# Optimization experiments

Measured on AMD Instinct MI355X. Metric: run time of the kernel, lower is better.

## Reference

```python
import jax, jax.numpy as jnp
import numpy as np

NUM_HEADS = 16
NEG_INF = -1e24


def setup_inputs() -> dict:
    key = jax.random.key(0)
    k1, k2, k3, k4 = jax.random.split(key, 4)
    T, B, E = 2048, 2, 1024
    std = 0.02
    return {
        "x": jax.random.normal(k1, (T, B, E), dtype=jnp.float32),
        "in_proj_weight": jax.random.normal(k2, (3 * E, E), dtype=jnp.float32) * std,
        "in_proj_bias": jnp.zeros((3 * E,), dtype=jnp.float32),
        "out_w": jax.random.normal(k3, (E, E), dtype=jnp.float32) * std,
        "out_b": jnp.zeros((E,), dtype=jnp.float32),
        "key_padding_mask": jax.random.randint(k4, (T, B), 0, 2) > 0,
    }


def reference(x, in_proj_weight, in_proj_bias, out_w, out_b, key_padding_mask):
    # x: [T, B, E]  (Time x Batch x Channel), self-attention (qkv_same path)
    T, B, E = x.shape
    H = NUM_HEADS
    hd = E // H
    scaling = hd ** -0.5
    qkv = jnp.einsum("tbe,fe->tbf", x, in_proj_weight) + in_proj_bias  # [T,B,3E]
    q, k, v = jnp.split(qkv, 3, axis=-1)
    q = (q * scaling).reshape(T, B, H, hd)
    k = k.reshape(T, B, H, hd)
    v = v.reshape(T, B, H, hd)
    # attention scores: [B, H, T(tgt), S(src)]
    scores = jnp.einsum("tbhd,sbhd->bhts", q, k)
    # key_padding_mask: [S, B] -> broadcast over [B, 1, 1, S]
    pad = key_padding_mask.T[:, None, None, :]
    scores = jnp.where(pad, jnp.float32(NEG_INF), scores)
    attn_weights = jax.nn.softmax(scores, axis=-1)
    # dropout p=0.0 in eval -> identity
    attn = jnp.einsum("bhts,sbhd->tbhd", attn_weights, v).reshape(T, B, E)
    out = jnp.einsum("tbe,fe->tbf", attn, out_w) + out_b
    return out
```

## Files before the change

### kernel.cpp

```cpp
#include <hip/hip_runtime.h>
#include <math.h>

#define T_    2048
#define B_    2
#define E_    1024
#define H_    16
#define HD_   64
#define KD_   1024
#define N3_   3072
#define M_    4096
#define NEGI  -1e24f

typedef __attribute__((ext_vector_type(8))) short          bf16x8;
typedef __attribute__((ext_vector_type(4))) float          f32x4;
typedef __attribute__((ext_vector_type(8))) unsigned short u16x8;

__device__ __forceinline__ unsigned short f2bf(float x) {
    unsigned int u = __float_as_uint(x);
    return (unsigned short)((u + 0x7fffu + ((u >> 16) & 1u)) >> 16);
}

__device__ __forceinline__ unsigned int cvtpk_bf16(float a, float b) {
    unsigned int r;
    asm("v_cvt_pk_bf16_f32 %0, %1, %2" : "=v"(r) : "v"(a), "v"(b));
    return r;
}

__device__ __forceinline__ void gload16(const unsigned short* g, unsigned short* s) {
    __builtin_amdgcn_global_load_lds(
        (const __attribute__((address_space(1))) void*)g,
        (__attribute__((address_space(3))) void*)s, 16, 0, 0);
}

#define XN4  ((size_t)M_ * KD_ / 4)
#define WIN4 ((size_t)N3_ * KD_ / 4)
#define WON4 ((size_t)E_ * KD_ / 4)
__global__ __launch_bounds__(256) void cvt_all(const float* __restrict__ x,
                                               const float* __restrict__ wi,
                                               const float* __restrict__ wo,
                                               unsigned short* __restrict__ dst) {
    const size_t i = (size_t)blockIdx.x * 256 + threadIdx.x;
    const float* s; size_t off;
    if (i < XN4)             { s = x;  off = i; }
    else if (i < XN4 + WIN4) { s = wi; off = i - XN4; }
    else                     { s = wo; off = i - XN4 - WIN4; }
    float4 v = ((const float4*)s)[off];
    ushort4 o;
    o.x = f2bf(v.x); o.y = f2bf(v.y); o.z = f2bf(v.z); o.w = f2bf(v.w);
    ((ushort4*)dst)[i] = o;
}

__global__ __launch_bounds__(256) void build_msk(const int* __restrict__ m,
                                                 float* __restrict__ o) {
    int i = blockIdx.x * 256 + threadIdx.x;
    if (i >= T_ * B_) return;
    o[(i & 1) * T_ + (i >> 1)] = m[i] ? NEGI : 0.f;
}

template <int EPI>
__global__ __launch_bounds__(256) void gemm_mfma(
    const unsigned short* __restrict__ A, const unsigned short* __restrict__ W,
    const float* __restrict__ bias,
    unsigned short* __restrict__ q_o, unsigned short* __restrict__ k_o,
    unsigned short* __restrict__ v_o, float* __restrict__ f_o)
{
    __shared__ __align__(16) unsigned short Ab[128 * 64];
    __shared__ __align__(16) unsigned short Bb[128 * 64];
    const int tid = threadIdx.x;
    const int l = tid & 63, w = tid >> 6;
    const int lr = l & 15, g = l >> 4;
    const int m0 = blockIdx.y * 128, n0 = blockIdx.x * 128;
    const int wr = (w >> 1) * 64, wc = (w & 1) * 64;

    f32x4 acc[4][4];
    #pragma unroll
    for (int i = 0; i < 4; ++i)
        #pragma unroll
        for (int j = 0; j < 4; ++j) acc[i][j] = f32x4{0.f, 0.f, 0.f, 0.f};

    for (int k0 = 0; k0 < KD_; k0 += 64) {
        __syncthreads();
        #pragma unroll
        for (int i = 0; i < 4; ++i) {
            const int fb  = (i * 4 + w) * 64;
            const int row = (fb + l) >> 3;
            const int col = ((l & 7) ^ (row & 7)) * 8;
            gload16(&A[(size_t)(m0 + row) * KD_ + k0 + col], &Ab[fb * 8]);
            gload16(&W[(size_t)(n0 + row) * KD_ + k0 + col], &Bb[fb * 8]);
        }
        __syncthreads();
        #pragma unroll
        for (int ks = 0; ks < 2; ++ks) {
            bf16x8 af[4], bf[4];
            #pragma unroll
            for (int mi = 0; mi < 4; ++mi) {
                const int row = wr + mi * 16 + lr;
                af[mi] = *(const bf16x8*)&Ab[row * 64 + (((ks * 4 + g) ^ (row & 7)) * 8)];
            }
            #pragma unroll
            for (int ni = 0; ni < 4; ++ni) {
                const int row = wc + ni * 16 + lr;
                bf[ni] = *(const bf16x8*)&Bb[row * 64 + (((ks * 4 + g) ^ (row & 7)) * 8)];
            }
            #pragma unroll
            for (int mi = 0; mi < 4; ++mi)
                #pragma unroll
                for (int ni = 0; ni < 4; ++ni)
                    acc[mi][ni] = __builtin_amdgcn_mfma_f32_16x16x32_bf16(
                        af[mi], bf[ni], acc[mi][ni], 0, 0, 0);
        }
    }

    if (EPI == 0) {
        const int sec = n0 >> 10;
        unsigned short* dst = (sec == 0) ? q_o : (sec == 1) ? k_o : v_o;
        const float sc = (sec == 0) ? 0.125f : 1.f;
        #pragma unroll
        for (int ni = 0; ni < 4; ++ni) {
            const int fcol = n0 + wc + ni * 16 + lr;
            const int h = (fcol >> 6) & 15, d = fcol & 63;
            const float bv = bias[fcol];
            #pragma unroll
            for (int mi = 0; mi < 4; ++mi)
                #pragma unroll
                for (int p = 0; p < 4; ++p) {
                    const int m = m0 + wr + mi * 16 + g * 4 + p;
                    const int t = m >> 1, b = m & 1;
                    dst[((size_t)(b * H_ + h) * T_ + t) * HD_ + d] =
                        f2bf((acc[mi][ni][p] + bv) * sc);
                }
        }
    } else {
        #pragma unroll
        for (int ni = 0; ni < 4; ++ni) {
            const int fcol = n0 + wc + ni * 16 + lr;
            const float bv = bias[fcol];
            #pragma unroll
            for (int mi = 0; mi < 4; ++mi)
                #pragma unroll
                for (int p = 0; p < 4; ++p) {
                    const int m = m0 + wr + mi * 16 + g * 4 + p;
                    f_o[(size_t)m * E_ + fcol] = acc[mi][ni][p] + bv;
                }
        }
    }
}

__global__ __launch_bounds__(256) void transpose64(const unsigned short* __restrict__ v,
                                                   unsigned short* __restrict__ vt)
{
    __shared__ __align__(16) unsigned short tile[64][72];
    const int bh = blockIdx.y, t0 = blockIdx.x * 64;
    const int tid = threadIdx.x;
    const int r = tid >> 2, c0 = (tid & 3) * 16;
    const unsigned short* src = v + ((size_t)bh * T_ + t0 + r) * HD_ + c0;
    *(u16x8*)&tile[r][c0]     = *(const u16x8*)&src[0];
    *(u16x8*)&tile[r][c0 + 8] = *(const u16x8*)&src[8];
    __syncthreads();
    u16x8 a, b;
    #pragma unroll
    for (int j = 0; j < 8; ++j) a[j] = tile[c0 + j][r];
    #pragma unroll
    for (int j = 0; j < 8; ++j) b[j] = tile[c0 + 8 + j][r];
    unsigned short* dq = vt + ((size_t)bh * HD_ + r) * T_ + t0 + c0;
    *(u16x8*)&dq[0] = a;
    *(u16x8*)&dq[8] = b;
}

__device__ __forceinline__ void stage8(const unsigned short* src, int ld,
                                       unsigned short* buf, int w, int l) {
    const int fb  = w * 64;
    const int row = (fb + l) >> 3;
    const int col = ((l & 7) ^ (row & 7)) * 8;
    gload16(src + (size_t)row * ld + col, buf + fb * 8);
}

__global__ __launch_bounds__(512, 2) void attn_mfma(
    const unsigned short* __restrict__ qw, const unsigned short* __restrict__ kw,
    const unsigned short* __restrict__ vtw, const float* __restrict__ msk,
    unsigned short* __restrict__ attn)
{
    __shared__ __align__(16) unsigned short Kb[2][64 * 64];
    __shared__ __align__(16) unsigned short Vb[2][64 * 64];
    __shared__ __align__(16) unsigned short Pb[8][32 * 64];

    const int tid = threadIdx.x;
    const int l = tid & 63, w = tid >> 6;
    const int lr = l & 15, g = l >> 4;
    const int bh = blockIdx.y, b = bh >> 4, h = bh & 15;
    const int q0 = blockIdx.x * 256 + w * 32;

    const unsigned short* kb  = kw  + (size_t)bh * T_ * HD_;
    const unsigned short* vtb = vtw + (size_t)bh * HD_ * T_;
    const float* mb = msk + b * T_;
    unsigned short* Pw = Pb[w];

    bf16x8 qf[2][2];
    #pragma unroll
    for (int qc = 0; qc < 2; ++qc) {
        const unsigned short* qrow = qw + ((size_t)bh * T_ + q0 + qc * 16 + lr) * HD_;
        qf[qc][0] = *(const bf16x8*)&qrow[g * 8];
        qf[qc][1] = *(const bf16x8*)&qrow[32 + g * 8];
    }

    f32x4 o[2][4];
    #pragma unroll
    for (int qc = 0; qc < 2; ++qc)
        #pragma unroll
        for (int df = 0; df < 4; ++df) o[qc][df] = f32x4{0.f, 0.f, 0.f, 0.f};
    float m_run[2] = {-INFINITY, -INFINITY}, l_run[2] = {0.f, 0.f};

    stage8(kb, HD_, Kb[0], w, l);
    stage8(vtb, T_, Vb[0], w, l);
    int cur = 0;

    for (int s0 = 0; s0 < T_; s0 += 64) {
        __syncthreads();
        if (s0 + 64 < T_) {
            stage8(kb + (size_t)(s0 + 64) * HD_, HD_, Kb[cur ^ 1], w, l);
            stage8(vtb + (s0 + 64),          T_, Vb[cur ^ 1], w, l);
        }
        const unsigned short* Kc = Kb[cur];
        const unsigned short* Vc = Vb[cur];

        f32x4 st[4][2];
        #pragma unroll
        for (int sf = 0; sf < 4; ++sf) {
            const int row = sf * 16 + lr;
            const bf16x8 k0v = *(const bf16x8*)&Kc[row * 64 + ((g       ^ (row & 7)) * 8)];
            const bf16x8 k1v = *(const bf16x8*)&Kc[row * 64 + (((4 + g) ^ (row & 7)) * 8)];
            #pragma unroll
            for (int qc = 0; qc < 2; ++qc) {
                f32x4 z = f32x4{0.f, 0.f, 0.f, 0.f};
                z           = __builtin_amdgcn_mfma_f32_16x16x32_bf16(k0v, qf[qc][0], z, 0, 0, 0);
                st[sf][qc]  = __builtin_amdgcn_mfma_f32_16x16x32_bf16(k1v, qf[qc][1], z, 0, 0, 0);
            }
        }
        float4 mv[4];
        #pragma unroll
        for (int sf = 0; sf < 4; ++sf) mv[sf] = *(const float4*)&mb[s0 + sf * 16 + g * 4];

        #pragma unroll
        for (int qc = 0; qc < 2; ++qc) {
            float pmax = -INFINITY;
            #pragma unroll
            for (int sf = 0; sf < 4; ++sf) {
                st[sf][qc][0] += mv[sf].x; st[sf][qc][1] += mv[sf].y;
                st[sf][qc][2] += mv[sf].z; st[sf][qc][3] += mv[sf].w;
                pmax = fmaxf(pmax, fmaxf(fmaxf(st[sf][qc][0], st[sf][qc][1]),
                                         fmaxf(st[sf][qc][2], st[sf][qc][3])));
            }
            pmax = fmaxf(pmax, __shfl_xor(pmax, 16));
            pmax = fmaxf(pmax, __shfl_xor(pmax, 32));
            if (!__all(pmax - m_run[qc] <= 8.f)) {
                const float mnew = fmaxf(m_run[qc], pmax);
                const float fac  = __expf(m_run[qc] - mnew);
                l_run[qc] *= fac;
                #pragma unroll
                for (int df = 0; df < 4; ++df) {
                    o[qc][df][0] *= fac; o[qc][df][1] *= fac;
                    o[qc][df][2] *= fac; o[qc][df][3] *= fac;
                }
                m_run[qc] = mnew;
            }
            const float mcur = m_run[qc];
            float rsum = 0.f;
            unsigned int pk[8];
            #pragma unroll
            for (int sf = 0; sf < 4; ++sf) {
                const float e0 = __expf(st[sf][qc][0] - mcur), e1 = __expf(st[sf][qc][1] - mcur);
                const float e2 = __expf(st[sf][qc][2] - mcur), e3 = __expf(st[sf][qc][3] - mcur);
                rsum += (e0 + e1) + (e2 + e3);
                pk[sf * 2 + 0] = cvtpk_bf16(e0, e1);
                pk[sf * 2 + 1] = cvtpk_bf16(e2, e3);
            }
            rsum += __shfl_xor(rsum, 16);
            rsum += __shfl_xor(rsum, 32);
            l_run[qc] += rsum;
            const int prow = qc * 16 + lr;
            #pragma unroll
            for (int sf = 0; sf < 4; ++sf) {
                const int blkS = (sf * 2 + (g >> 1)) ^ (prow & 7);
                uint2 val; val.x = pk[sf * 2]; val.y = pk[sf * 2 + 1];
                *(uint2*)&Pw[prow * 64 + blkS * 8 + (g & 1) * 4] = val;
            }
        }

        #pragma unroll
        for (int ks = 0; ks < 2; ++ks) {
            bf16x8 pf[2];
            #pragma unroll
            for (int qc = 0; qc < 2; ++qc) {
                const int prow = qc * 16 + lr;
                pf[qc] = *(const bf16x8*)&Pw[prow * 64 + (((ks * 4 + g) ^ (prow & 7)) * 8)];
            }
            #pragma unroll
            for (int df = 0; df < 4; ++df) {
                const int vrow = df * 16 + lr;
                const bf16x8 vf = *(const bf16x8*)&Vc[vrow * 64 + (((ks * 4 + g) ^ (vrow & 7)) * 8)];
                #pragma unroll
                for (int qc = 0; qc < 2; ++qc)
                    o[qc][df] = __builtin_amdgcn_mfma_f32_16x16x32_bf16(vf, pf[qc], o[qc][df], 0, 0, 0);
            }
        }
        cur ^= 1;
    }

    #pragma unroll
    for (int qc = 0; qc < 2; ++qc) {
        const float inv = 1.f / l_run[qc];
        const int t = q0 + qc * 16 + lr;
        #pragma unroll
        for (int df = 0; df < 4; ++df) {
            ushort4 ov;
            ov.x = f2bf(o[qc][df][0] * inv); ov.y = f2bf(o[qc][df][1] * inv);
            ov.z = f2bf(o[qc][df][2] * inv); ov.w = f2bf(o[qc][df][3] * inv);
            *(ushort4*)&attn[((size_t)t * B_ + b) * E_ + h * HD_ + df * 16 + g * 4] = ov;
        }
    }
}

extern "C" void kernel_launch(void* const* d_in, const int* in_sizes, int n_in,
                              void* d_out, int out_size, void* d_ws, size_t ws_size,
                              hipStream_t stream)
{
    const float* x     = (const float*)d_in[0];
    const float* w_in  = (const float*)d_in[1];
    const float* b_in  = (const float*)d_in[2];
    const float* w_out = (const float*)d_in[3];
    const float* b_out = (const float*)d_in[4];
    const int*   mask  = (const int*)d_in[5];

    const size_t NX = (size_t)M_ * KD_;
    unsigned short* xb   = (unsigned short*)d_ws;
    unsigned short* wib  = xb  + NX;
    unsigned short* wob  = wib + (size_t)N3_ * KD_;
    unsigned short* qb   = wob + (size_t)E_ * KD_;
    unsigned short* kbuf = qb   + NX;
    unsigned short* vbuf = kbuf + NX;
    unsigned short* vtb  = vbuf + NX;
    float*          mskf = (float*)(vtb + NX);
    unsigned short* attnb = xb;

    const int cvt_blocks = (int)((XN4 + WIN4 + WON4) / 256);
    cvt_all  <<<cvt_blocks,        256, 0, stream>>>(x, w_in, w_out, xb);
    build_msk<<<(T_*B_ + 255)/256, 256, 0, stream>>>(mask, mskf);

    gemm_mfma<0><<<dim3(N3_/128, M_/128), 256, 0, stream>>>(xb, wib, b_in, qb, kbuf, vbuf, nullptr);
    transpose64 <<<dim3(T_/64, B_*H_),    256, 0, stream>>>(vbuf, vtb);
    attn_mfma   <<<dim3(T_/256, B_*H_),   512, 0, stream>>>(qb, kbuf, vtb, mskf, attnb);
    gemm_mfma<1><<<dim3(E_/128, M_/128),  256, 0, stream>>>(attnb, wob, b_out,
                                                            nullptr, nullptr, nullptr, (float*)d_out);
}
```

Measured before the change: 230.8 us.

## Load K/V fragments directly into registers with register double-buffering, drop LDS staging

The attention kernel no longer stages K and V tiles through shared memory with block-wide barriers. Each wave now loads its MFMA fragments straight from global memory into a pair of register buffers, prefetching the next tile while computing the current one, and wraps the MFMA phases in s_setprio. This removes the __syncthreads and LDS traffic for K/V. The cost is that every wave in the block reloads the same K/V from global/L2 (8x redundancy) and register pressure rises, which may hurt occupancy under launch_bounds(512,2).

New measurement: 283.7 us. +22.9%, slower.

```diff
diff --git a/kernel.cpp b/kernel.cpp
--- a/kernel.cpp
+++ b/kernel.cpp
@@ -167,12 +167,115 @@
     *(u16x8*)&dq[8] = b;
 }
 
-__device__ __forceinline__ void stage8(const unsigned short* src, int ld,
-                                       unsigned short* buf, int w, int l) {
-    const int fb  = w * 64;
-    const int row = (fb + l) >> 3;
-    const int col = ((l & 7) ^ (row & 7)) * 8;
-    gload16(src + (size_t)row * ld + col, buf + fb * 8);
+struct KVreg { bf16x8 k[4][2]; bf16x8 v[4][2]; };
+
+__device__ __forceinline__ void load_kf(const unsigned short* kb, int s, int lr, int g,
+                                        KVreg& r) {
+    #pragma unroll
+    for (int sf = 0; sf < 4; ++sf)
+        #pragma unroll
+        for (int hh = 0; hh < 2; ++hh)
+            r.k[sf][hh] = *(const bf16x8*)&kb[(size_t)(s + sf * 16 + lr) * HD_ + hh * 32 + g * 8];
+}
+__device__ __forceinline__ void load_vf(const unsigned short* vtb, int s, int lr, int g,
+                                        KVreg& r) {
+    #pragma unroll
+    for (int df = 0; df < 4; ++df)
+        #pragma unroll
+        for (int ks = 0; ks < 2; ++ks)
+            r.v[df][ks] = *(const bf16x8*)&vtb[(size_t)(df * 16 + lr) * T_ + s + ks * 32 + g * 8];
+}
+
+__device__ __forceinline__ void attn_tile(
+    int s0, int sn, KVreg& cur, KVreg& nxt,
+    const unsigned short* kb, const unsigned short* vtb,
+    const float* mb, unsigned short* Pw,
+    const bf16x8 (&qf)[2][2], float (&m_run)[2], float (&l_run)[2], f32x4 (&o)[2][4],
+    int lr, int g)
+{
+    load_kf(kb, sn, lr, g, nxt);
+
+    f32x4 st[4][2];
+    __builtin_amdgcn_s_setprio(1);
+    #pragma unroll
+    for (int sf = 0; sf < 4; ++sf)
+        #pragma unroll
+        for (int qc = 0; qc < 2; ++qc) {
+            f32x4 z = f32x4{0.f, 0.f, 0.f, 0.f};
+            z          = __builtin_amdgcn_mfma_f32_16x16x32_bf16(cur.k[sf][0], qf[qc][0], z, 0, 0, 0);
+            st[sf][qc] = __builtin_amdgcn_mfma_f32_16x16x32_bf16(cur.k[sf][1], qf[qc][1], z, 0, 0, 0);
+        }
+    __builtin_amdgcn_s_setprio(0);
+
+    load_vf(vtb, sn, lr, g, nxt);
+
+    float4 mv[4];
+    #pragma unroll
+    for (int sf = 0; sf < 4; ++sf) mv[sf] = *(const float4*)&mb[s0 + sf * 16 + g * 4];
+
+    #pragma unroll
+    for (int qc = 0; qc < 2; ++qc) {
+        float pmax = -INFINITY;
+        #pragma unroll
+        for (int sf = 0; sf < 4; ++sf) {
+            st[sf][qc][0] += mv[sf].x; st[sf][qc][1] += mv[sf].y;
+            st[sf][qc][2] += mv[sf].z; st[sf][qc][3] += mv[sf].w;
+            pmax = fmaxf(pmax, fmaxf(fmaxf(st[sf][qc][0], st[sf][qc][1]),
+                                     fmaxf(st[sf][qc][2], st[sf][qc][3])));
+        }
+        pmax = fmaxf(pmax, __shfl_xor(pmax, 16));
+        pmax = fmaxf(pmax, __shfl_xor(pmax, 32));
+        if (!__all(pmax - m_run[qc] <= 8.f)) {
+            const float mnew = fmaxf(m_run[qc], pmax);
+            const float fac  = __expf(m_run[qc] - mnew);
+            l_run[qc] *= fac;
+            #pragma unroll
+            for (int df = 0; df < 4; ++df) {
+                o[qc][df][0] *= fac; o[qc][df][1] *= fac;
+                o[qc][df][2] *= fac; o[qc][df][3] *= fac;
+            }
+            m_run[qc] = mnew;
+        }
+        const float mcur = m_run[qc];
+        float rsum = 0.f;
+        unsigned int pk[8];
+        #pragma unroll
+        for (int sf = 0; sf < 4; ++sf) {
+            const float e0 = __expf(st[sf][qc][0] - mcur), e1 = __expf(st[sf][qc][1] - mcur);
+            const float e2 = __expf(st[sf][qc][2] - mcur), e3 = __expf(st[sf][qc][3] - mcur);
+            rsum += (e0 + e1) + (e2 + e3);
+            pk[sf * 2 + 0] = cvtpk_bf16(e0, e1);
+            pk[sf * 2 + 1] = cvtpk_bf16(e2, e3);
+        }
+        rsum += __shfl_xor(rsum, 16);
+        rsum += __shfl_xor(rsum, 32);
+        l_run[qc] += rsum;
+        const int prow = qc * 16 + lr;
+        #pragma unroll
+        for (int sf = 0; sf < 4; ++sf) {
+            const int blkS = (sf * 2 + (g >> 1)) ^ (prow & 7);
+            uint2 val; val.x = pk[sf * 2]; val.y = pk[sf * 2 + 1];
+            *(uint2*)&Pw[prow * 64 + blkS * 8 + (g & 1) * 4] = val;
+        }
+    }
+
+    __builtin_amdgcn_s_setprio(1);
+    #pragma unroll
+    for (int ks = 0; ks < 2; ++ks) {
+        bf16x8 pf[2];
+        #pragma unroll
+        for (int qc = 0; qc < 2; ++qc) {
+            const int prow = qc * 16 + lr;
+            pf[qc] = *(const bf16x8*)&Pw[prow * 64 + (((ks * 4 + g) ^ (prow & 7)) * 8)];
+        }
+        #pragma unroll
+        for (int df = 0; df < 4; ++df)
+            #pragma unroll
+            for (int qc = 0; qc < 2; ++qc)
+                o[qc][df] = __builtin_amdgcn_mfma_f32_16x16x32_bf16(
+                    cur.v[df][ks], pf[qc], o[qc][df], 0, 0, 0);
+    }
+    __builtin_amdgcn_s_setprio(0);
 }
 
 __global__ __launch_bounds__(512, 2) void attn_mfma(
@@ -180,8 +283,6 @@
     const unsigned short* __restrict__ vtw, const float* __restrict__ msk,
     unsigned short* __restrict__ attn)
 {
-    __shared__ __align__(16) unsigned short Kb[2][64 * 64];
-    __shared__ __align__(16) unsigned short Vb[2][64 * 64];
     __shared__ __align__(16) unsigned short Pb[8][32 * 64];
 
     const int tid = threadIdx.x;
@@ -210,100 +311,14 @@
         for (int df = 0; df < 4; ++df) o[qc][df] = f32x4{0.f, 0.f, 0.f, 0.f};
     float m_run[2] = {-INFINITY, -INFINITY}, l_run[2] = {0.f, 0.f};
 
-    stage8(kb, HD_, Kb[0], w, l);
-    stage8(vtb, T_, Vb[0], w, l);
-    int cur = 0;
-
-    for (int s0 = 0; s0 < T_; s0 += 64) {
-        __syncthreads();
-        if (s0 + 64 < T_) {
-            stage8(kb + (size_t)(s0 + 64) * HD_, HD_, Kb[cur ^ 1], w, l);
-            stage8(vtb + (s0 + 64),          T_, Vb[cur ^ 1], w, l);
-        }
-        const unsigned short* Kc = Kb[cur];
-        const unsigned short* Vc = Vb[cur];
-
-        f32x4 st[4][2];
-        #pragma unroll
-        for (int sf = 0; sf < 4; ++sf) {
-            const int row = sf * 16 + lr;
-            const bf16x8 k0v = *(const bf16x8*)&Kc[row * 64 + ((g       ^ (row & 7)) * 8)];
-            const bf16x8 k1v = *(const bf16x8*)&Kc[row * 64 + (((4 + g) ^ (row & 7)) * 8)];
-            #pragma unroll
-            for (int qc = 0; qc < 2; ++qc) {
-                f32x4 z = f32x4{0.f, 0.f, 0.f, 0.f};
-                z           = __builtin_amdgcn_mfma_f32_16x16x32_bf16(k0v, qf[qc][0], z, 0, 0, 0);
-                st[sf][qc]  = __builtin_amdgcn_mfma_f32_16x16x32_bf16(k1v, qf[qc][1], z, 0, 0, 0);
-            }
-        }
-        float4 mv[4];
-        #pragma unroll
-        for (int sf = 0; sf < 4; ++sf) mv[sf] = *(const float4*)&mb[s0 + sf * 16 + g * 4];
-
-        #pragma unroll
-        for (int qc = 0; qc < 2; ++qc) {
-            float pmax = -INFINITY;
-            #pragma unroll
-            for (int sf = 0; sf < 4; ++sf) {
-                st[sf][qc][0] += mv[sf].x; st[sf][qc][1] += mv[sf].y;
-                st[sf][qc][2] += mv[sf].z; st[sf][qc][3] += mv[sf].w;
-                pmax = fmaxf(pmax, fmaxf(fmaxf(st[sf][qc][0], st[sf][qc][1]),
-                                         fmaxf(st[sf][qc][2], st[sf][qc][3])));
-            }
-            pmax = fmaxf(pmax, __shfl_xor(pmax, 16));
-            pmax = fmaxf(pmax, __shfl_xor(pmax, 32));
-            if (!__all(pmax - m_run[qc] <= 8.f)) {
-                const float mnew = fmaxf(m_run[qc], pmax);
-                const float fac  = __expf(m_run[qc] - mnew);
-                l_run[qc] *= fac;
-                #pragma unroll
-                for (int df = 0; df < 4; ++df) {
-                    o[qc][df][0] *= fac; o[qc][df][1] *= fac;
-                    o[qc][df][2] *= fac; o[qc][df][3] *= fac;
-                }
-                m_run[qc] = mnew;
-            }
-            const float mcur = m_run[qc];
-            float rsum = 0.f;
-            unsigned int pk[8];
-            #pragma unroll
-            for (int sf = 0; sf < 4; ++sf) {
-                const float e0 = __expf(st[sf][qc][0] - mcur), e1 = __expf(st[sf][qc][1] - mcur);
-                const float e2 = __expf(st[sf][qc][2] - mcur), e3 = __expf(st[sf][qc][3] - mcur);
-                rsum += (e0 + e1) + (e2 + e3);
-                pk[sf * 2 + 0] = cvtpk_bf16(e0, e1);
-                pk[sf * 2 + 1] = cvtpk_bf16(e2, e3);
-            }
-            rsum += __shfl_xor(rsum, 16);
-            rsum += __shfl_xor(rsum, 32);
-            l_run[qc] += rsum;
-            const int prow = qc * 16 + lr;
-            #pragma unroll
-            for (int sf = 0; sf < 4; ++sf) {
-                const int blkS = (sf * 2 + (g >> 1)) ^ (prow & 7);
-                uint2 val; val.x = pk[sf * 2]; val.y = pk[sf * 2 + 1];
-                *(uint2*)&Pw[prow * 64 + blkS * 8 + (g & 1) * 4] = val;
-            }
-        }
-
-        #pragma unroll
-        for (int ks = 0; ks < 2; ++ks) {
-            bf16x8 pf[2];
-            #pragma unroll
-            for (int qc = 0; qc < 2; ++qc) {
-                const int prow = qc * 16 + lr;
-                pf[qc] = *(const bf16x8*)&Pw[prow * 64 + (((ks * 4 + g) ^ (prow & 7)) * 8)];
-            }
-            #pragma unroll
-            for (int df = 0; df < 4; ++df) {
-                const int vrow = df * 16 + lr;
-                const bf16x8 vf = *(const bf16x8*)&Vc[vrow * 64 + (((ks * 4 + g) ^ (vrow & 7)) * 8)];
-                #pragma unroll
-                for (int qc = 0; qc < 2; ++qc)
-                    o[qc][df] = __builtin_amdgcn_mfma_f32_16x16x32_bf16(vf, pf[qc], o[qc][df], 0, 0, 0);
-            }
-        }
-        cur ^= 1;
+    KVreg rA, rB;
+    load_kf(kb, 0, lr, g, rA);
+    load_vf(vtb, 0, lr, g, rA);
+
+    for (int s0 = 0; s0 < T_; s0 += 128) {
+        const int s2 = (s0 + 128 < T_) ? s0 + 128 : s0;
+        attn_tile(s0,      s0 + 64, rA, rB, kb, vtb, mb, Pw, qf, m_run, l_run, o, lr, g);
+        attn_tile(s0 + 64, s2,      rB, rA, kb, vtb, mb, Pw, qf, m_run, l_run, o, lr, g);
     }
 
     #pragma unroll
```

## Fuse mask build into convert, write V transposed in GEMM, load V from global

Applied to the files above, without the earlier changes.

The mask construction now runs as extra blocks of the conversion kernel. The QKV GEMM epilogue writes V directly in transposed layout, which removes the separate transpose kernel and its buffer. The attention kernel drops V staging in LDS and instead loads V fragments straight from global memory into registers. It also raises the occupancy hint to 4 blocks per CU. The aim is fewer launches and less LDS traffic, at the cost of strided scattered stores in the GEMM epilogue and uncached global V loads inside the attention loop.

Measured after the change: 320.8 us. 1.39x slower.

```diff
diff --git a/kernel.cpp b/kernel.cpp
--- a/kernel.cpp
+++ b/kernel.cpp
@@ -35,10 +35,18 @@
 #define XN4  ((size_t)M_ * KD_ / 4)
 #define WIN4 ((size_t)N3_ * KD_ / 4)
 #define WON4 ((size_t)E_ * KD_ / 4)
+#define CVTB 8192
 __global__ __launch_bounds__(256) void cvt_all(const float* __restrict__ x,
                                                const float* __restrict__ wi,
                                                const float* __restrict__ wo,
-                                               unsigned short* __restrict__ dst) {
+                                               unsigned short* __restrict__ dst,
+                                               const int* __restrict__ m,
+                                               float* __restrict__ mskf) {
+    if (blockIdx.x >= CVTB) {
+        const int i = (blockIdx.x - CVTB) * 256 + threadIdx.x;
+        if (i < T_ * B_) mskf[(i & 1) * T_ + (i >> 1)] = m[i] ? NEGI : 0.f;
+        return;
+    }
     const size_t i = (size_t)blockIdx.x * 256 + threadIdx.x;
     const float* s; size_t off;
     if (i < XN4)             { s = x;  off = i; }
@@ -50,19 +58,12 @@
     ((ushort4*)dst)[i] = o;
 }
 
-__global__ __launch_bounds__(256) void build_msk(const int* __restrict__ m,
-                                                 float* __restrict__ o) {
-    int i = blockIdx.x * 256 + threadIdx.x;
-    if (i >= T_ * B_) return;
-    o[(i & 1) * T_ + (i >> 1)] = m[i] ? NEGI : 0.f;
-}
-
 template <int EPI>
 __global__ __launch_bounds__(256) void gemm_mfma(
     const unsigned short* __restrict__ A, const unsigned short* __restrict__ W,
     const float* __restrict__ bias,
     unsigned short* __restrict__ q_o, unsigned short* __restrict__ k_o,
-    unsigned short* __restrict__ v_o, float* __restrict__ f_o)
+    unsigned short* __restrict__ vt_o, float* __restrict__ f_o)
 {
     __shared__ __align__(16) unsigned short Ab[128 * 64];
     __shared__ __align__(16) unsigned short Bb[128 * 64];
@@ -113,7 +114,6 @@
 
     if (EPI == 0) {
         const int sec = n0 >> 10;
-        unsigned short* dst = (sec == 0) ? q_o : (sec == 1) ? k_o : v_o;
         const float sc = (sec == 0) ? 0.125f : 1.f;
         #pragma unroll
         for (int ni = 0; ni < 4; ++ni) {
@@ -126,8 +126,13 @@
                 for (int p = 0; p < 4; ++p) {
                     const int m = m0 + wr + mi * 16 + g * 4 + p;
                     const int t = m >> 1, b = m & 1;
-                    dst[((size_t)(b * H_ + h) * T_ + t) * HD_ + d] =
-                        f2bf((acc[mi][ni][p] + bv) * sc);
+                    const unsigned short val = f2bf((acc[mi][ni][p] + bv) * sc);
+                    if (sec == 0)
+                        q_o[((size_t)(b * H_ + h) * T_ + t) * HD_ + d] = val;
+                    else if (sec == 1)
+                        k_o[((size_t)(b * H_ + h) * T_ + t) * HD_ + d] = val;
+                    else
+                        vt_o[((size_t)(b * H_ + h) * HD_ + d) * T_ + t] = val;
                 }
         }
     } else {
@@ -146,42 +151,20 @@
     }
 }
 
-__global__ __launch_bounds__(256) void transpose64(const unsigned short* __restrict__ v,
-                                                   unsigned short* __restrict__ vt)
-{
-    __shared__ __align__(16) unsigned short tile[64][72];
-    const int bh = blockIdx.y, t0 = blockIdx.x * 64;
-    const int tid = threadIdx.x;
-    const int r = tid >> 2, c0 = (tid & 3) * 16;
-    const unsigned short* src = v + ((size_t)bh * T_ + t0 + r) * HD_ + c0;
-    *(u16x8*)&tile[r][c0]     = *(const u16x8*)&src[0];
-    *(u16x8*)&tile[r][c0 + 8] = *(const u16x8*)&src[8];
-    __syncthreads();
-    u16x8 a, b;
-    #pragma unroll
-    for (int j = 0; j < 8; ++j) a[j] = tile[c0 + j][r];
-    #pragma unroll
-    for (int j = 0; j < 8; ++j) b[j] = tile[c0 + 8 + j][r];
-    unsigned short* dq = vt + ((size_t)bh * HD_ + r) * T_ + t0 + c0;
-    *(u16x8*)&dq[0] = a;
-    *(u16x8*)&dq[8] = b;
-}
-
-__device__ __forceinline__ void stage8(const unsigned short* src, int ld,
+__device__ __forceinline__ void stage8(const unsigned short* src,
                                        unsigned short* buf, int w, int l) {
     const int fb  = w * 64;
     const int row = (fb + l) >> 3;
     const int col = ((l & 7) ^ (row & 7)) * 8;
-    gload16(src + (size_t)row * ld + col, buf + fb * 8);
-}
-
-__global__ __launch_bounds__(512, 2) void attn_mfma(
+    gload16(src + (size_t)row * HD_ + col, buf + fb * 8);
+}
+
+__global__ __launch_bounds__(512, 4) void attn_mfma(
     const unsigned short* __restrict__ qw, const unsigned short* __restrict__ kw,
     const unsigned short* __restrict__ vtw, const float* __restrict__ msk,
     unsigned short* __restrict__ attn)
 {
     __shared__ __align__(16) unsigned short Kb[2][64 * 64];
-    __shared__ __align__(16) unsigned short Vb[2][64 * 64];
     __shared__ __align__(16) unsigned short Pb[8][32 * 64];
 
     const int tid = threadIdx.x;
@@ -210,19 +193,21 @@
         for (int df = 0; df < 4; ++df) o[qc][df] = f32x4{0.f, 0.f, 0.f, 0.f};
     float m_run[2] = {-INFINITY, -INFINITY}, l_run[2] = {0.f, 0.f};
 
-    stage8(kb, HD_, Kb[0], w, l);
-    stage8(vtb, T_, Vb[0], w, l);
+    stage8(kb, Kb[0], w, l);
     int cur = 0;
 
     for (int s0 = 0; s0 < T_; s0 += 64) {
         __syncthreads();
-        if (s0 + 64 < T_) {
-            stage8(kb + (size_t)(s0 + 64) * HD_, HD_, Kb[cur ^ 1], w, l);
-            stage8(vtb + (s0 + 64),          T_, Vb[cur ^ 1], w, l);
-        }
+
+        bf16x8 vf0[4];
+        #pragma unroll
+        for (int df = 0; df < 4; ++df)
+            vf0[df] = *(const bf16x8*)&vtb[(size_t)(df * 16 + lr) * T_ + s0 + g * 8];
+
+        if (s0 + 64 < T_)
+            stage8(kb + (size_t)(s0 + 64) * HD_, Kb[cur ^ 1], w, l);
+
         const unsigned short* Kc = Kb[cur];
-        const unsigned short* Vc = Vb[cur];
-
         f32x4 st[4][2];
         #pragma unroll
         for (int sf = 0; sf < 4; ++sf) {
@@ -236,6 +221,12 @@
                 st[sf][qc]  = __builtin_amdgcn_mfma_f32_16x16x32_bf16(k1v, qf[qc][1], z, 0, 0, 0);
             }
         }
+
+        bf16x8 vf1[4];
+        #pragma unroll
+        for (int df = 0; df < 4; ++df)
+            vf1[df] = *(const bf16x8*)&vtb[(size_t)(df * 16 + lr) * T_ + s0 + 32 + g * 8];
+
         float4 mv[4];
         #pragma unroll
         for (int sf = 0; sf < 4; ++sf) mv[sf] = *(const float4*)&mb[s0 + sf * 16 + g * 4];
@@ -296,11 +287,11 @@
             }
             #pragma unroll
             for (int df = 0; df < 4; ++df) {
-                const int vrow = df * 16 + lr;
-                const bf16x8 vf = *(const bf16x8*)&Vc[vrow * 64 + (((ks * 4 + g) ^ (vrow & 7)) * 8)];
+                const bf16x8 vv = (ks == 0) ? vf0[df] : vf1[df];
                 #pragma unroll
                 for (int qc = 0; qc < 2; ++qc)
-                    o[qc][df] = __builtin_amdgcn_mfma_f32_16x16x32_bf16(vf, pf[qc], o[qc][df], 0, 0, 0);
+                    o[qc][df] = __builtin_amdgcn_mfma_f32_16x16x32_bf16(
+                        vv, pf[qc], o[qc][df], 0, 0, 0);
             }
         }
         cur ^= 1;
@@ -337,17 +328,13 @@
     unsigned short* wob  = wib + (size_t)N3_ * KD_;
     unsigned short* qb   = wob + (size_t)E_ * KD_;
     unsigned short* kbuf = qb   + NX;
-    unsigned short* vbuf = kbuf + NX;
-    unsigned short* vtb  = vbuf + NX;
+    unsigned short* vtb  = kbuf + NX;
     float*          mskf = (float*)(vtb + NX);
     unsigned short* attnb = xb;
 
-    const int cvt_blocks = (int)((XN4 + WIN4 + WON4) / 256);
-    cvt_all  <<<cvt_blocks,        256, 0, stream>>>(x, w_in, w_out, xb);
-    build_msk<<<(T_*B_ + 255)/256, 256, 0, stream>>>(mask, mskf);
-
-    gemm_mfma<0><<<dim3(N3_/128, M_/128), 256, 0, stream>>>(xb, wib, b_in, qb, kbuf, vbuf, nullptr);
-    transpose64 <<<dim3(T_/64, B_*H_),    256, 0, stream>>>(vbuf, vtb);
+    cvt_all<<<CVTB + 16, 256, 0, stream>>>(x, w_in, w_out, xb, mask, mskf);
+
+    gemm_mfma<0><<<dim3(N3_/128, M_/128), 256, 0, stream>>>(xb, wib, b_in, qb, kbuf, vtb, nullptr);
     attn_mfma   <<<dim3(T_/256, B_*H_),   512, 0, stream>>>(qb, kbuf, vtb, mskf, attnb);
     gemm_mfma<1><<<dim3(E_/128, M_/128),  256, 0, stream>>>(attnb, wob, b_out,
                                                             nullptr, nullptr, nullptr, (float*)d_out);
```

## Give each attention wave 64 query rows and fold mask build into convert kernel

Applied to the files above, without the earlier changes.

The attention kernel now runs 256 threads (4 waves) per block, with each wave owning 64 query rows instead of 32. K fragments are loaded from LDS once per tile and reused across four query chunks, which halves LDS K/V reads per unit of MFMA work. Separately, the mask-building kernel is merged into the fp32-to-bf16 convert kernel as 16 extra blocks, removing one launch. In exchange, per-thread register use roughly doubles (accumulators and Q fragments), and the grid keeps the same 256 blocks with fewer waves per block, which may lower occupancy and latency hiding.

Result: slower. 247.4 us (+7.2%).

```diff
diff --git a/kernel.cpp b/kernel.cpp
--- a/kernel.cpp
+++ b/kernel.cpp
@@ -35,10 +35,18 @@
 #define XN4  ((size_t)M_ * KD_ / 4)
 #define WIN4 ((size_t)N3_ * KD_ / 4)
 #define WON4 ((size_t)E_ * KD_ / 4)
+#define CVTB 8192
 __global__ __launch_bounds__(256) void cvt_all(const float* __restrict__ x,
                                                const float* __restrict__ wi,
                                                const float* __restrict__ wo,
-                                               unsigned short* __restrict__ dst) {
+                                               unsigned short* __restrict__ dst,
+                                               const int* __restrict__ m,
+                                               float* __restrict__ mskf) {
+    if (blockIdx.x >= CVTB) {
+        const int i = (blockIdx.x - CVTB) * 256 + threadIdx.x;
+        if (i < T_ * B_) mskf[(i & 1) * T_ + (i >> 1)] = m[i] ? NEGI : 0.f;
+        return;
+    }
     const size_t i = (size_t)blockIdx.x * 256 + threadIdx.x;
     const float* s; size_t off;
     if (i < XN4)             { s = x;  off = i; }
@@ -48,13 +56,6 @@
     ushort4 o;
     o.x = f2bf(v.x); o.y = f2bf(v.y); o.z = f2bf(v.z); o.w = f2bf(v.w);
     ((ushort4*)dst)[i] = o;
-}
-
-__global__ __launch_bounds__(256) void build_msk(const int* __restrict__ m,
-                                                 float* __restrict__ o) {
-    int i = blockIdx.x * 256 + threadIdx.x;
-    if (i >= T_ * B_) return;
-    o[(i & 1) * T_ + (i >> 1)] = m[i] ? NEGI : 0.f;
 }
 
 template <int EPI>
@@ -167,88 +168,93 @@
     *(u16x8*)&dq[8] = b;
 }
 
-__device__ __forceinline__ void stage8(const unsigned short* src, int ld,
+__device__ __forceinline__ void stage4(const unsigned short* src, int ld,
                                        unsigned short* buf, int w, int l) {
-    const int fb  = w * 64;
-    const int row = (fb + l) >> 3;
-    const int col = ((l & 7) ^ (row & 7)) * 8;
-    gload16(src + (size_t)row * ld + col, buf + fb * 8);
-}
-
-__global__ __launch_bounds__(512, 2) void attn_mfma(
+    #pragma unroll
+    for (int c = 0; c < 2; ++c) {
+        const int fb  = (c * 4 + w) * 64;
+        const int row = (fb + l) >> 3;
+        const int col = ((l & 7) ^ (row & 7)) * 8;
+        gload16(src + (size_t)row * ld + col, buf + fb * 8);
+    }
+}
+
+__global__ __launch_bounds__(256) void attn_mfma(
     const unsigned short* __restrict__ qw, const unsigned short* __restrict__ kw,
     const unsigned short* __restrict__ vtw, const float* __restrict__ msk,
     unsigned short* __restrict__ attn)
 {
     __shared__ __align__(16) unsigned short Kb[2][64 * 64];
     __shared__ __align__(16) unsigned short Vb[2][64 * 64];
-    __shared__ __align__(16) unsigned short Pb[8][32 * 64];
+    __shared__ __align__(16) unsigned short Pb[4][64 * 64];
 
     const int tid = threadIdx.x;
     const int l = tid & 63, w = tid >> 6;
     const int lr = l & 15, g = l >> 4;
     const int bh = blockIdx.y, b = bh >> 4, h = bh & 15;
-    const int q0 = blockIdx.x * 256 + w * 32;
+    const int q0 = blockIdx.x * 256 + w * 64;
 
     const unsigned short* kb  = kw  + (size_t)bh * T_ * HD_;
     const unsigned short* vtb = vtw + (size_t)bh * HD_ * T_;
     const float* mb = msk + b * T_;
     unsigned short* Pw = Pb[w];
 
-    bf16x8 qf[2][2];
-    #pragma unroll
-    for (int qc = 0; qc < 2; ++qc) {
+    bf16x8 qf[4][2];
+    #pragma unroll
+    for (int qc = 0; qc < 4; ++qc) {
         const unsigned short* qrow = qw + ((size_t)bh * T_ + q0 + qc * 16 + lr) * HD_;
         qf[qc][0] = *(const bf16x8*)&qrow[g * 8];
         qf[qc][1] = *(const bf16x8*)&qrow[32 + g * 8];
     }
 
-    f32x4 o[2][4];
-    #pragma unroll
-    for (int qc = 0; qc < 2; ++qc)
+    f32x4 o[4][4];
+    #pragma unroll
+    for (int qc = 0; qc < 4; ++qc)
         #pragma unroll
         for (int df = 0; df < 4; ++df) o[qc][df] = f32x4{0.f, 0.f, 0.f, 0.f};
-    float m_run[2] = {-INFINITY, -INFINITY}, l_run[2] = {0.f, 0.f};
-
-    stage8(kb, HD_, Kb[0], w, l);
-    stage8(vtb, T_, Vb[0], w, l);
+    float m_run[4] = {-INFINITY, -INFINITY, -INFINITY, -INFINITY};
+    float l_run[4] = {0.f, 0.f, 0.f, 0.f};
+
+    stage4(kb, HD_, Kb[0], w, l);
+    stage4(vtb, T_, Vb[0], w, l);
     int cur = 0;
 
     for (int s0 = 0; s0 < T_; s0 += 64) {
         __syncthreads();
         if (s0 + 64 < T_) {
-            stage8(kb + (size_t)(s0 + 64) * HD_, HD_, Kb[cur ^ 1], w, l);
-            stage8(vtb + (s0 + 64),          T_, Vb[cur ^ 1], w, l);
+            stage4(kb + (size_t)(s0 + 64) * HD_, HD_, Kb[cur ^ 1], w, l);
+            stage4(vtb + (s0 + 64),          T_, Vb[cur ^ 1], w, l);
         }
         const unsigned short* Kc = Kb[cur];
         const unsigned short* Vc = Vb[cur];
 
-        f32x4 st[4][2];
+        bf16x8 kv[4][2];
         #pragma unroll
         for (int sf = 0; sf < 4; ++sf) {
             const int row = sf * 16 + lr;
-            const bf16x8 k0v = *(const bf16x8*)&Kc[row * 64 + ((g       ^ (row & 7)) * 8)];
-            const bf16x8 k1v = *(const bf16x8*)&Kc[row * 64 + (((4 + g) ^ (row & 7)) * 8)];
-            #pragma unroll
-            for (int qc = 0; qc < 2; ++qc) {
+            kv[sf][0] = *(const bf16x8*)&Kc[row * 64 + ((g       ^ (row & 7)) * 8)];
+            kv[sf][1] = *(const bf16x8*)&Kc[row * 64 + (((4 + g) ^ (row & 7)) * 8)];
+        }
+        float4 mv[4];
+        #pragma unroll
+        for (int sf = 0; sf < 4; ++sf) mv[sf] = *(const float4*)&mb[s0 + sf * 16 + g * 4];
+
+        #pragma unroll
+        for (int qc = 0; qc < 4; ++qc) {
+            f32x4 st[4];
+            #pragma unroll
+            for (int sf = 0; sf < 4; ++sf) {
                 f32x4 z = f32x4{0.f, 0.f, 0.f, 0.f};
-                z           = __builtin_amdgcn_mfma_f32_16x16x32_bf16(k0v, qf[qc][0], z, 0, 0, 0);
-                st[sf][qc]  = __builtin_amdgcn_mfma_f32_16x16x32_bf16(k1v, qf[qc][1], z, 0, 0, 0);
-            }
-        }
-        float4 mv[4];
-        #pragma unroll
-        for (int sf = 0; sf < 4; ++sf) mv[sf] = *(const float4*)&mb[s0 + sf * 16 + g * 4];
-
-        #pragma unroll
-        for (int qc = 0; qc < 2; ++qc) {
+                z      = __builtin_amdgcn_mfma_f32_16x16x32_bf16(kv[sf][0], qf[qc][0], z, 0, 0, 0);
+                st[sf] = __builtin_amdgcn_mfma_f32_16x16x32_bf16(kv[sf][1], qf[qc][1], z, 0, 0, 0);
+            }
             float pmax = -INFINITY;
             #pragma unroll
             for (int sf = 0; sf < 4; ++sf) {
-                st[sf][qc][0] += mv[sf].x; st[sf][qc][1] += mv[sf].y;
-                st[sf][qc][2] += mv[sf].z; st[sf][qc][3] += mv[sf].w;
-                pmax = fmaxf(pmax, fmaxf(fmaxf(st[sf][qc][0], st[sf][qc][1]),
-                                         fmaxf(st[sf][qc][2], st[sf][qc][3])));
+                st[sf][0] += mv[sf].x; st[sf][1] += mv[sf].y;
+                st[sf][2] += mv[sf].z; st[sf][3] += mv[sf].w;
+                pmax = fmaxf(pmax, fmaxf(fmaxf(st[sf][0], st[sf][1]),
+                                         fmaxf(st[sf][2], st[sf][3])));
             }
             pmax = fmaxf(pmax, __shfl_xor(pmax, 16));
             pmax = fmaxf(pmax, __shfl_xor(pmax, 32));
@@ -268,8 +274,8 @@
             unsigned int pk[8];
             #pragma unroll
             for (int sf = 0; sf < 4; ++sf) {
-                const float e0 = __expf(st[sf][qc][0] - mcur), e1 = __expf(st[sf][qc][1] - mcur);
-                const float e2 = __expf(st[sf][qc][2] - mcur), e3 = __expf(st[sf][qc][3] - mcur);
+                const float e0 = __expf(st[sf][0] - mcur), e1 = __expf(st[sf][1] - mcur);
+                const float e2 = __expf(st[sf][2] - mcur), e3 = __expf(st[sf][3] - mcur);
                 rsum += (e0 + e1) + (e2 + e3);
                 pk[sf * 2 + 0] = cvtpk_bf16(e0, e1);
                 pk[sf * 2 + 1] = cvtpk_bf16(e2, e3);
@@ -288,9 +294,9 @@
 
         #pragma unroll
         for (int ks = 0; ks < 2; ++ks) {
-            bf16x8 pf[2];
-            #pragma unroll
-            for (int qc = 0; qc < 2; ++qc) {
+            bf16x8 pf[4];
+            #pragma unroll
+            for (int qc = 0; qc < 4; ++qc) {
                 const int prow = qc * 16 + lr;
                 pf[qc] = *(const bf16x8*)&Pw[prow * 64 + (((ks * 4 + g) ^ (prow & 7)) * 8)];
             }
@@ -299,7 +305,7 @@
                 const int vrow = df * 16 + lr;
                 const bf16x8 vf = *(const bf16x8*)&Vc[vrow * 64 + (((ks * 4 + g) ^ (vrow & 7)) * 8)];
                 #pragma unroll
-                for (int qc = 0; qc < 2; ++qc)
+                for (int qc = 0; qc < 4; ++qc)
                     o[qc][df] = __builtin_amdgcn_mfma_f32_16x16x32_bf16(vf, pf[qc], o[qc][df], 0, 0, 0);
             }
         }
@@ -307,7 +313,7 @@
     }
 
     #pragma unroll
-    for (int qc = 0; qc < 2; ++qc) {
+    for (int qc = 0; qc < 4; ++qc) {
         const float inv = 1.f / l_run[qc];
         const int t = q0 + qc * 16 + lr;
         #pragma unroll
@@ -342,13 +348,11 @@
     float*          mskf = (float*)(vtb + NX);
     unsigned short* attnb = xb;
 
-    const int cvt_blocks = (int)((XN4 + WIN4 + WON4) / 256);
-    cvt_all  <<<cvt_blocks,        256, 0, stream>>>(x, w_in, w_out, xb);
-    build_msk<<<(T_*B_ + 255)/256, 256, 0, stream>>>(mask, mskf);
+    cvt_all<<<CVTB + 16, 256, 0, stream>>>(x, w_in, w_out, xb, mask, mskf);
 
     gemm_mfma<0><<<dim3(N3_/128, M_/128), 256, 0, stream>>>(xb, wib, b_in, qb, kbuf, vbuf, nullptr);
     transpose64 <<<dim3(T_/64, B_*H_),    256, 0, stream>>>(vbuf, vtb);
-    attn_mfma   <<<dim3(T_/256, B_*H_),   512, 0, stream>>>(qb, kbuf, vtb, mskf, attnb);
+    attn_mfma   <<<dim3(T_/256, B_*H_),   256, 0, stream>>>(qb, kbuf, vtb, mskf, attnb);
     gemm_mfma<1><<<dim3(E_/128, M_/128),  256, 0, stream>>>(attnb, wob, b_out,
                                                             nullptr, nullptr, nullptr, (float*)d_out);
 }
```
